# Kernel optimization log

Measured on AMD Instinct MI355X. Metric: run time of the kernel, lower is better.

Reference implementation:

```python
import jax, jax.numpy as jnp
import numpy as np

B, N, DIM = 1, 100_000, 512
HEADS, DIM_HEAD, M = 8, 64, 64


def setup_inputs() -> dict:
    key = jax.random.key(0)
    ks = jax.random.split(key, 9)
    s = 0.04  # ~ kaiming-ish scale for dim=512
    return {
        "x": jax.random.normal(ks[0], (B, N, DIM), dtype=jnp.float32),
        "temperature": jnp.full((1, HEADS, 1, 1), 0.5, dtype=jnp.float32),
        "w_slice": jax.random.normal(ks[1], (HEADS * M, DIM), dtype=jnp.float32) * s,
        "b_slice": jnp.zeros((HEADS * M,), dtype=jnp.float32),
        "w1": jax.random.normal(ks[2], (DIM_HEAD, DIM), dtype=jnp.float32) * s,
        "b1": jnp.zeros((DIM_HEAD,), dtype=jnp.float32),
        "wq": jax.random.normal(ks[3], (DIM_HEAD, DIM_HEAD), dtype=jnp.float32) * 0.125,
        "wk": jax.random.normal(ks[4], (DIM_HEAD, DIM_HEAD), dtype=jnp.float32) * 0.125,
        "wv": jax.random.normal(ks[5], (DIM_HEAD, DIM_HEAD), dtype=jnp.float32) * 0.125,
        "w3": jax.random.normal(ks[6], (DIM_HEAD, DIM_HEAD), dtype=jnp.float32) * 0.125,
        "b3": jnp.zeros((DIM_HEAD,), dtype=jnp.float32),
    }


def reference(x, temperature, w_slice, b_slice, w1, b1, wq, wk, wv, w3, b3):
    b, n, c = x.shape
    # slice logits: (B,N,H*M) -> (B,H,N,M)
    logits = jnp.einsum("bnc,ec->bne", x, w_slice) + b_slice
    logits = logits.reshape(b, n, HEADS, M).transpose(0, 2, 1, 3)
    temp = jnp.clip(temperature, 0.1, 5.0)
    w = jax.nn.softmax(logits / temp, axis=-1)          # (B,H,N,M)
    d = w.sum(axis=2)                                    # (B,H,M)
    # N -> M aggregation (w^T @ x per head)
    s_raw = jnp.einsum("bhnm,bnc->bhmc", w, x)          # (B,H,M,C)
    s = jnp.einsum("bhmc,dc->bhmd", s_raw / (d[..., None] + 1e-5), w1) + b1  # (B,H,M,dh)
    q = jnp.einsum("bhmd,ed->bhme", s, wq)
    k = jnp.einsum("bhmd,ed->bhme", s, wk)
    v = jnp.einsum("bhmd,ed->bhme", s, wv)
    scale = 1.0 / jnp.sqrt(jnp.asarray(DIM_HEAD, dtype=s.dtype))
    attn = jax.nn.softmax(jnp.einsum("bhme,bhle->bhml", q, k) * scale, axis=-1)
    s_att = jnp.einsum("bhml,bhle->bhme", attn, v)      # (B,H,M,dh)
    s_out = jnp.einsum("bhme,de->bhmd", s_att, w3) + b3
    # deslice: w @ s_out -> (B,H,N,dh) -> (B,N,H*dh)
    x_out = jnp.einsum("bhnm,bhmd->bhnd", w, s_out)
    return x_out.transpose(0, 2, 1, 3).reshape(b, n, HEADS * DIM_HEAD)
```

## Files before the change

### kernel.cpp

```cpp
#include <hip/hip_runtime.h>

typedef _Float16 f16;
typedef _Float16 f16x8 __attribute__((ext_vector_type(8)));
typedef _Float16 f16x4 __attribute__((ext_vector_type(4)));
typedef float    f32x4 __attribute__((ext_vector_type(4)));

#define N_TOK   100000
#define NPAD    100032
#define NT1     1563
#define CDIM    512
#define KSTEPS  (NPAD/32)
#define K2SPL   128

#define O_WT     ((size_t)0)
#define SZ_WT    ((size_t)512*NPAD*2)
#define O_YT     (O_WT + SZ_WT)
#define SZ_YT    ((size_t)64*NPAD*2)
#define O_WFR    (O_YT + SZ_YT)
#define SZ_WFR   ((size_t)16*4*9*64*8*2)
#define O_SPP    (O_WFR + SZ_WFR)
#define SZ_SPP   ((size_t)K2SPL*32768*4)
#define O_DPP    (O_SPP + SZ_SPP)
#define SZ_DPP   ((size_t)K2SPL*512*4)
#define O_SPRE   (O_DPP + SZ_DPP)
#define SZ_SPRE  ((size_t)32768*4)
#define O_DSTD   (O_SPRE + SZ_SPRE)
#define SZ_DSTD  ((size_t)512*4)
#define O_SOUT   (O_DSTD + SZ_DSTD)
#define SZ_SOUT  ((size_t)8*64*64*2)
#define O_WN     (O_SOUT + SZ_SOUT)
#define SZ_WN    ((size_t)NPAD*512*2)

__global__ void k0_pack(const float* __restrict__ wsf, const float* __restrict__ w1f,
                        f16* __restrict__ wfr) {
    int c = blockIdx.x * 256 + threadIdx.x;
    int lane = c & 63, g = c >> 6;
    int u  = g % 9,  r = g / 9;
    int we = r & 3,  kg = r >> 2;
    int col = lane & 15, quad = lane >> 4;
    int k = kg * 32 + quad * 8;
    const float* src;
    if (u < 8) src = wsf + (size_t)(we*128 + u*16 + col) * CDIM + k;
    else       src = w1f + (size_t)(we*16  + col) * CDIM + k;
    float4 a = *(const float4*)(src);
    float4 b = *(const float4*)(src + 4);
    f16x8 h;
    h[0]=(f16)a.x; h[1]=(f16)a.y; h[2]=(f16)a.z; h[3]=(f16)a.w;
    h[4]=(f16)b.x; h[5]=(f16)b.y; h[6]=(f16)b.z; h[7]=(f16)b.w;
    *(f16x8*)(wfr + (size_t)c * 8) = h;
}

#define XROW 40
#define TPITCH 72
#define NPITCH 536
__launch_bounds__(256, 2)
__global__ void k1_slice(const float* __restrict__ x, const float* __restrict__ temperature,
                         const f16* __restrict__ wfr, const float* __restrict__ bsl,
                         f16* __restrict__ wT, f16* __restrict__ yT, f16* __restrict__ wN) {
    __shared__ f16 smem[512 * TPITCH];
    f16* lX = smem;
    f16* lT = smem;
    f16* lN = smem;

    const int tid  = threadIdx.x;
    const int wave = tid >> 6;
    const int lane = tid & 63;
    const int quad = lane >> 4;
    const int col  = lane & 15;
    const int n0   = blockIdx.x * 64;

    const int srow = tid >> 2, sch = tid & 3;
    int snr = n0 + srow; if (snr > N_TOK - 1) snr = N_TOK - 1;
    const float* sbase = x + (size_t)snr * CDIM + sch * 8;

    {
        float4 a = *(const float4*)(sbase);
        float4 b = *(const float4*)(sbase + 4);
        f16x8 h;
        h[0]=(f16)a.x; h[1]=(f16)a.y; h[2]=(f16)a.z; h[3]=(f16)a.w;
        h[4]=(f16)b.x; h[5]=(f16)b.y; h[6]=(f16)b.z; h[7]=(f16)b.w;
        *(f16x8*)(&lX[srow * XROW + sch * 8]) = h;
    }

    f32x4 acc[4][9];
    #pragma unroll
    for (int nf = 0; nf < 4; ++nf)
        #pragma unroll
        for (int u = 0; u < 9; ++u) acc[nf][u] = f32x4{0.f,0.f,0.f,0.f};

    __syncthreads();

    #pragma unroll 2
    for (int kg = 0; kg < 16; ++kg) {
        const f16* wb = wfr + ((size_t)(kg*4 + wave) * 9) * 512 + (size_t)lane * 8;
        f16x8 bf[9];
        #pragma unroll
        for (int u = 0; u < 9; ++u) bf[u] = *(const f16x8*)(wb + u * 512);

        float4 xa, xb;
        if (kg < 15) {
            xa = *(const float4*)(sbase + (kg + 1) * 32);
            xb = *(const float4*)(sbase + (kg + 1) * 32 + 4);
        }

        const f16* xbuf = lX + (kg & 1) * (64 * XROW);
        f16x8 af[4];
        #pragma unroll
        for (int nf = 0; nf < 4; ++nf)
            af[nf] = *(const f16x8*)(xbuf + (nf*16 + col) * XROW + quad * 8);

        #pragma unroll
        for (int nf = 0; nf < 4; ++nf)
            #pragma unroll
            for (int u = 0; u < 9; ++u)
                acc[nf][u] = __builtin_amdgcn_mfma_f32_16x16x32_f16(af[nf], bf[u], acc[nf][u], 0, 0, 0);

        if (kg < 15) {
            f16x8 h;
            h[0]=(f16)xa.x; h[1]=(f16)xa.y; h[2]=(f16)xa.z; h[3]=(f16)xa.w;
            h[4]=(f16)xb.x; h[5]=(f16)xb.y; h[6]=(f16)xb.z; h[7]=(f16)xb.w;
            *(f16x8*)(&lX[((kg + 1) & 1) * (64 * XROW) + srow * XROW + sch * 8]) = h;
        }
        __syncthreads();
    }

    #pragma unroll
    for (int u = 0; u < 8; ++u) {
        float b = bsl[wave*128 + u*16 + col];
        #pragma unroll
        for (int nf = 0; nf < 4; ++nf)
            #pragma unroll
            for (int r = 0; r < 4; ++r) acc[nf][u][r] += b;
    }
    float invt[2];
    #pragma unroll
    for (int hh = 0; hh < 2; ++hh) {
        float tv = temperature[wave*2 + hh];
        tv = fminf(fmaxf(tv, 0.1f), 5.0f);
        invt[hh] = 1.0f / tv;
    }

    #pragma unroll
    for (int nf = 0; nf < 4; ++nf) {
        const int nloc = nf*16 + quad*4;
        #pragma unroll
        for (int hh = 0; hh < 2; ++hh) {
            float mx[4];
            #pragma unroll
            for (int r = 0; r < 4; ++r) {
                float m01 = fmaxf(acc[nf][hh*4+0][r], acc[nf][hh*4+1][r]);
                float m23 = fmaxf(acc[nf][hh*4+2][r], acc[nf][hh*4+3][r]);
                mx[r] = fmaxf(m01, m23);
            }
            #pragma unroll
            for (int d = 1; d < 16; d <<= 1)
                #pragma unroll
                for (int r = 0; r < 4; ++r) mx[r] = fmaxf(mx[r], __shfl_xor(mx[r], d));
            float sm[4] = {0.f, 0.f, 0.f, 0.f};
            #pragma unroll
            for (int uu = 0; uu < 4; ++uu)
                #pragma unroll
                for (int r = 0; r < 4; ++r) {
                    float ev = __expf((acc[nf][hh*4+uu][r] - mx[r]) * invt[hh]);
                    acc[nf][hh*4+uu][r] = ev;
                    sm[r] += ev;
                }
            #pragma unroll
            for (int d = 1; d < 16; d <<= 1)
                #pragma unroll
                for (int r = 0; r < 4; ++r) sm[r] += __shfl_xor(sm[r], d);
            #pragma unroll
            for (int r = 0; r < 4; ++r) sm[r] = 1.0f / sm[r];
            #pragma unroll
            for (int uu = 0; uu < 4; ++uu) {
                f16x4 pk;
                #pragma unroll
                for (int r = 0; r < 4; ++r) {
                    acc[nf][hh*4+uu][r] *= sm[r];
                    int n = n0 + nloc + r;
                    pk[r] = (n < N_TOK) ? (f16)acc[nf][hh*4+uu][r] : (f16)0.f;
                }
                int e = wave*128 + (hh*4 + uu)*16 + col;
                *(f16x4*)(lT + (size_t)e*TPITCH + nloc) = pk;
            }
        }
        {
            f16x4 pk;
            #pragma unroll
            for (int r = 0; r < 4; ++r) {
                int n = n0 + nloc + r;
                pk[r] = (n < N_TOK) ? (f16)acc[nf][8][r] : (f16)0.f;
            }
            *(f16x4*)(yT + (size_t)(wave*16 + col) * NPAD + n0 + nloc) = pk;
        }
    }
    __syncthreads();

    #pragma unroll
    for (int i = 0; i < 16; ++i) {
        int id = tid + i*256;
        int e = id >> 3, p = id & 7;
        f16x8 v = *(const f16x8*)(lT + (size_t)e*TPITCH + p*8);
        *(f16x8*)(wT + (size_t)e*NPAD + n0 + p*8) = v;
    }

    if (wN != nullptr) {
        __syncthreads();
        #pragma unroll
        for (int nf = 0; nf < 4; ++nf) {
            const int nloc = nf*16 + quad*4;
            #pragma unroll
            for (int hh = 0; hh < 2; ++hh)
                #pragma unroll
                for (int uu = 0; uu < 4; ++uu) {
                    int e = wave*128 + (hh*4 + uu)*16 + col;
                    #pragma unroll
                    for (int r = 0; r < 4; ++r)
                        lN[(size_t)(nloc + r)*NPITCH + e] = (f16)acc[nf][hh*4+uu][r];
                }
        }
        __syncthreads();
        #pragma unroll
        for (int i = 0; i < 16; ++i) {
            int id = tid + i*256;
            int n = id >> 6, ec = id & 63;
            f16x8 v = *(const f16x8*)(lN + (size_t)n*NPITCH + ec*8);
            *(f16x8*)(wN + (size_t)(n0 + n)*512 + ec*8) = v;
        }
    }
}

__launch_bounds__(256, 4)
__global__ void k2_spre(const f16* __restrict__ wT, const f16* __restrict__ yT,
                        float* __restrict__ spp, float* __restrict__ dpp) {
    const int tid = threadIdx.x, wave = tid >> 6, lane = tid & 63;
    const int quad = lane >> 4, col = lane & 15;
    const int slot = blockIdx.x >> 2, equad = blockIdx.x & 3;
    const int ebase = equad * 128 + wave * 32;

    f32x4 acc[2][4];
    float dac[2];
    #pragma unroll
    for (int u = 0; u < 2; ++u) {
        dac[u] = 0.f;
        #pragma unroll
        for (int v = 0; v < 4; ++v) acc[u][v] = f32x4{0.f,0.f,0.f,0.f};
    }
    for (int ks = slot; ks < KSTEPS; ks += K2SPL) {
        int nb = ks*32 + quad*8;
        f16x8 bf[4];
        #pragma unroll
        for (int v = 0; v < 4; ++v)
            bf[v] = *(const f16x8*)(yT + (size_t)(v*16 + col)*NPAD + nb);
        #pragma unroll
        for (int u = 0; u < 2; ++u) {
            f16x8 af = *(const f16x8*)(wT + (size_t)(ebase + u*16 + col)*NPAD + nb);
            #pragma unroll
            for (int v = 0; v < 4; ++v)
                acc[u][v] = __builtin_amdgcn_mfma_f32_16x16x32_f16(af, bf[v], acc[u][v], 0, 0, 0);
            float s = 0.f;
            #pragma unroll
            for (int j = 0; j < 8; ++j) s += (float)af[j];
            dac[u] += s;
        }
    }
    #pragma unroll
    for (int u = 0; u < 2; ++u) {
        dac[u] += __shfl_xor(dac[u], 16);
        dac[u] += __shfl_xor(dac[u], 32);
    }
    if (quad == 0) {
        #pragma unroll
        for (int u = 0; u < 2; ++u)
            dpp[slot*512 + ebase + u*16 + col] = dac[u];
    }
    float* dst = spp + (size_t)slot * 32768 + (size_t)equad * 8192;
    #pragma unroll
    for (int u = 0; u < 2; ++u)
        #pragma unroll
        for (int v = 0; v < 4; ++v)
            *(f32x4*)(dst + (size_t)((wave*2 + u)*4 + v)*256 + (size_t)lane*4) = acc[u][v];
}

__global__ void k2r_reduce(const float* __restrict__ spp, const float* __restrict__ dpp,
                           float* __restrict__ spre, float* __restrict__ dstd) {
    int i = blockIdx.x*256 + threadIdx.x;
    float s = 0.f;
    for (int p = 0; p < K2SPL; ++p) s += spp[(size_t)p*32768 + i];
    int r = i & 3, L = (i >> 2) & 63, v = (i >> 8) & 3, g = (i >> 10) & 7, eq = (i >> 13) & 3;
    int e = eq*128 + (g >> 1)*32 + (g & 1)*16 + (L >> 4)*4 + r;
    int d = v*16 + (L & 15);
    spre[e*64 + d] = s;
    if (i < 512) {
        float tt = 0.f;
        for (int p = 0; p < K2SPL; ++p) tt += dpp[p*512 + i];
        dstd[i] = tt;
    }
}

__global__ void k3_attn(const float* __restrict__ spre, const float* __restrict__ dstd,
                        const float* __restrict__ b1, const float* __restrict__ wq,
                        const float* __restrict__ wk, const float* __restrict__ wv,
                        const float* __restrict__ w3, const float* __restrict__ b3,
                        f16* __restrict__ sout) {
    __shared__ float wa[64][65], wb[64][65], wc[64][65];
    __shared__ float ss[64][65], qq[64][65], kk[64][65], vv[64][65], sc[64][65];
    const int h = blockIdx.x, tid = threadIdx.x;

    for (int i = tid; i < 4096; i += 1024) {
        int r = i >> 6, c = i & 63;
        wa[r][c] = wq[i];
        wb[r][c] = wk[i];
        wc[r][c] = wv[i];
        ss[r][c] = spre[h*4096 + i] / (dstd[h*64 + r] + 1e-5f) + b1[c];
    }
    __syncthreads();

    #pragma unroll
    for (int it = 0; it < 4; ++it) {
        int m = it*16 + (tid >> 6), e = tid & 63;
        float aq = 0.f, ak = 0.f, av = 0.f;
        #pragma unroll 8
        for (int d = 0; d < 64; ++d) {
            float sv = ss[m][d];
            aq += sv * wa[e][d];
            ak += sv * wb[e][d];
            av += sv * wc[e][d];
        }
        qq[m][e] = aq; kk[m][e] = ak; vv[m][e] = av;
    }
    __syncthreads();

    for (int i = tid; i < 4096; i += 1024) wa[i >> 6][i & 63] = w3[i];
    #pragma unroll
    for (int it = 0; it < 4; ++it) {
        int m = it*16 + (tid >> 6), l = tid & 63;
        float a = 0.f;
        #pragma unroll 8
        for (int e = 0; e < 64; ++e) a += qq[m][e] * kk[l][e];
        sc[m][l] = a * 0.125f;
    }
    __syncthreads();

    if (tid < 64) {
        int m = tid;
        float mx = -1e30f;
        #pragma unroll 8
        for (int l = 0; l < 64; ++l) mx = fmaxf(mx, sc[m][l]);
        float sm = 0.f;
        #pragma unroll 8
        for (int l = 0; l < 64; ++l) { float ev = __expf(sc[m][l] - mx); sc[m][l] = ev; sm += ev; }
        float rs = 1.0f / sm;
        #pragma unroll 8
        for (int l = 0; l < 64; ++l) sc[m][l] *= rs;
    }
    __syncthreads();

    #pragma unroll
    for (int it = 0; it < 4; ++it) {
        int m = it*16 + (tid >> 6), e = tid & 63;
        float a = 0.f;
        #pragma unroll 8
        for (int l = 0; l < 64; ++l) a += sc[m][l] * vv[l][e];
        ss[m][e] = a;
    }
    __syncthreads();

    #pragma unroll
    for (int it = 0; it < 4; ++it) {
        int d = it*16 + (tid >> 6), m = tid & 63;
        float a = b3[d];
        #pragma unroll 8
        for (int e = 0; e < 64; ++e) a += ss[m][e] * wa[d][e];
        sout[(h*64 + d)*64 + m] = (f16)a;
    }
}

__launch_bounds__(256, 3)
__global__ void k4_wn(const f16* __restrict__ wN, const f16* __restrict__ sout,
                      float* __restrict__ out) {
    const int tid = threadIdx.x, wave = tid >> 6, lane = tid & 63;
    const int quad = lane >> 4, col = lane & 15;
    const int n0 = blockIdx.x * 32;

    f32x4 acc[2][2][4];
    #pragma unroll
    for (int hh = 0; hh < 2; ++hh)
        #pragma unroll
        for (int t = 0; t < 2; ++t)
            #pragma unroll
            for (int v = 0; v < 4; ++v) acc[hh][t][v] = f32x4{0.f,0.f,0.f,0.f};

    #pragma unroll
    for (int hh = 0; hh < 2; ++hh) {
        int h = wave*2 + hh;
        #pragma unroll
        for (int ks = 0; ks < 2; ++ks) {
            f16x8 af[2], bf[4];
            #pragma unroll
            for (int t = 0; t < 2; ++t)
                af[t] = *(const f16x8*)(wN + (size_t)(n0 + t*16 + col)*512 + h*64 + ks*32 + quad*8);
            #pragma unroll
            for (int v = 0; v < 4; ++v)
                bf[v] = *(const f16x8*)(sout + (size_t)(h*64 + v*16 + col)*64 + ks*32 + quad*8);
            #pragma unroll
            for (int t = 0; t < 2; ++t)
                #pragma unroll
                for (int v = 0; v < 4; ++v)
                    acc[hh][t][v] = __builtin_amdgcn_mfma_f32_16x16x32_f16(af[t], bf[v], acc[hh][t][v], 0, 0, 0);
        }
    }

    #pragma unroll
    for (int hh = 0; hh < 2; ++hh) {
        int h = wave*2 + hh;
        #pragma unroll
        for (int t = 0; t < 2; ++t)
            #pragma unroll
            for (int v = 0; v < 4; ++v)
                #pragma unroll
                for (int r = 0; r < 4; ++r) {
                    int n = n0 + t*16 + quad*4 + r;
                    if (n < N_TOK)
                        out[(size_t)n*512 + h*64 + v*16 + col] = acc[hh][t][v][r];
                }
    }
}

__launch_bounds__(256, 2)
__global__ void k4_deslice(const f16* __restrict__ wT, const f16* __restrict__ sout,
                           float* __restrict__ out) {
    __shared__ f16 ldsW[512*68];
    const int tid = threadIdx.x, wave = tid >> 6, lane = tid & 63;
    const int quad = lane >> 4, col = lane & 15;
    const int n0 = blockIdx.x * 64;

    #pragma unroll
    for (int i = 0; i < 32; ++i) {
        int id = tid + i*256;
        int e = id >> 4, p = id & 15;
        f16x4 v = *(const f16x4*)(wT + (size_t)e*NPAD + n0 + p*4);
        *(f16x4*)(ldsW + (size_t)e*68 + p*4) = v;
    }
    __syncthreads();

    f32x4 acc[2][4][4];
    #pragma unroll
    for (int hh = 0; hh < 2; ++hh)
        #pragma unroll
        for (int t = 0; t < 4; ++t)
            #pragma unroll
            for (int v = 0; v < 4; ++v) acc[hh][t][v] = f32x4{0.f,0.f,0.f,0.f};

    #pragma unroll
    for (int hh = 0; hh < 2; ++hh) {
        int h = wave*2 + hh;
        #pragma unroll
        for (int ks = 0; ks < 2; ++ks) {
            f16x8 af[4];
            #pragma unroll
            for (int t = 0; t < 4; ++t) {
                f16x8 a;
                #pragma unroll
                for (int j = 0; j < 8; ++j)
                    a[j] = ldsW[(size_t)(h*64 + ks*32 + quad*8 + j)*68 + t*16 + col];
                af[t] = a;
            }
            #pragma unroll
            for (int v = 0; v < 4; ++v) {
                f16x8 bf = *(const f16x8*)(sout + (size_t)(h*64 + v*16 + col)*64 + ks*32 + quad*8);
                #pragma unroll
                for (int t = 0; t < 4; ++t)
                    acc[hh][t][v] = __builtin_amdgcn_mfma_f32_16x16x32_f16(af[t], bf, acc[hh][t][v], 0, 0, 0);
            }
        }
    }

    #pragma unroll
    for (int hh = 0; hh < 2; ++hh) {
        int h = wave*2 + hh;
        #pragma unroll
        for (int t = 0; t < 4; ++t)
            #pragma unroll
            for (int v = 0; v < 4; ++v)
                #pragma unroll
                for (int r = 0; r < 4; ++r) {
                    int n = n0 + t*16 + quad*4 + r;
                    if (n < N_TOK)
                        out[(size_t)n*512 + h*64 + v*16 + col] = acc[hh][t][v][r];
                }
    }
}

extern "C" void kernel_launch(void* const* d_in, const int* in_sizes, int n_in,
                              void* d_out, int out_size, void* d_ws, size_t ws_size,
                              hipStream_t stream) {
    const float* x           = (const float*)d_in[0];
    const float* temperature = (const float*)d_in[1];
    const float* w_slice     = (const float*)d_in[2];
    const float* b_slice     = (const float*)d_in[3];
    const float* w1          = (const float*)d_in[4];
    const float* b1          = (const float*)d_in[5];
    const float* wq          = (const float*)d_in[6];
    const float* wk          = (const float*)d_in[7];
    const float* wv          = (const float*)d_in[8];
    const float* w3          = (const float*)d_in[9];
    const float* b3          = (const float*)d_in[10];
    float* out = (float*)d_out;
    char*  ws  = (char*)d_ws;

    f16*   wT    = (f16*)(ws + O_WT);
    f16*   yT    = (f16*)(ws + O_YT);
    f16*   wfr   = (f16*)(ws + O_WFR);
    float* spp   = (float*)(ws + O_SPP);
    float* dpp   = (float*)(ws + O_DPP);
    float* spre  = (float*)(ws + O_SPRE);
    float* dstd  = (float*)(ws + O_DSTD);
    f16*   sout  = (f16*)(ws + O_SOUT);

    const int use_wn = (ws_size >= (O_WN + SZ_WN)) ? 1 : 0;
    f16* wN = use_wn ? (f16*)(ws + O_WN) : nullptr;

    k0_pack<<<144, 256, 0, stream>>>(w_slice, w1, wfr);
    k1_slice<<<NT1, 256, 0, stream>>>(x, temperature, wfr, b_slice, wT, yT, wN);
    k2_spre<<<K2SPL*4, 256, 0, stream>>>(wT, yT, spp, dpp);
    k2r_reduce<<<128, 256, 0, stream>>>(spp, dpp, spre, dstd);
    k3_attn<<<8, 1024, 0, stream>>>(spre, dstd, b1, wq, wk, wv, w3, b3, sout);
    if (use_wn) k4_wn<<<KSTEPS, 256, 0, stream>>>(wN, sout, out);
    else        k4_deslice<<<NT1, 256, 0, stream>>>(wT, sout, out);
}
```

Baseline: 634.8 us.

## Stage full x tile in LDS, software-pipeline k2, shrink k3 block, retune k4 bounds

k1 now loads the whole 64x512 x tile into shared memory up front, replacing the per-k-step double buffer and removing 16 barriers from the MFMA loop. k2 switches from strided k-step assignment to contiguous chunks per slot and double-buffers its global loads around the MFMAs. k3 runs with 256 threads instead of 1024, and k4 raises its launch-bounds occupancy hint. The larger LDS footprint in k1 fits within the existing 512x72 buffer but removes overlap of x loads with compute, and the tighter k4 register budget may cause spills.

```diff
diff --git a/kernel.cpp b/kernel.cpp
--- a/kernel.cpp
+++ b/kernel.cpp
@@ -50,7 +50,7 @@
     *(f16x8*)(wfr + (size_t)c * 8) = h;
 }
 
-#define XROW 40
+#define XPITCH 520
 #define TPITCH 72
 #define NPITCH 536
 __launch_bounds__(256, 2)
@@ -72,14 +72,14 @@
     const int srow = tid >> 2, sch = tid & 3;
     int snr = n0 + srow; if (snr > N_TOK - 1) snr = N_TOK - 1;
     const float* sbase = x + (size_t)snr * CDIM + sch * 8;
-
-    {
-        float4 a = *(const float4*)(sbase);
-        float4 b = *(const float4*)(sbase + 4);
+    #pragma unroll
+    for (int kg = 0; kg < 16; ++kg) {
+        float4 a = *(const float4*)(sbase + kg * 32);
+        float4 b = *(const float4*)(sbase + kg * 32 + 4);
         f16x8 h;
         h[0]=(f16)a.x; h[1]=(f16)a.y; h[2]=(f16)a.z; h[3]=(f16)a.w;
         h[4]=(f16)b.x; h[5]=(f16)b.y; h[6]=(f16)b.z; h[7]=(f16)b.w;
-        *(f16x8*)(&lX[srow * XROW + sch * 8]) = h;
+        *(f16x8*)(&lX[srow * XPITCH + kg * 32 + sch * 8]) = h;
     }
 
     f32x4 acc[4][9];
@@ -97,31 +97,16 @@
         #pragma unroll
         for (int u = 0; u < 9; ++u) bf[u] = *(const f16x8*)(wb + u * 512);
 
-        float4 xa, xb;
-        if (kg < 15) {
-            xa = *(const float4*)(sbase + (kg + 1) * 32);
-            xb = *(const float4*)(sbase + (kg + 1) * 32 + 4);
-        }
-
-        const f16* xbuf = lX + (kg & 1) * (64 * XROW);
         f16x8 af[4];
         #pragma unroll
         for (int nf = 0; nf < 4; ++nf)
-            af[nf] = *(const f16x8*)(xbuf + (nf*16 + col) * XROW + quad * 8);
+            af[nf] = *(const f16x8*)(&lX[(nf*16 + col) * XPITCH + kg * 32 + quad * 8]);
 
         #pragma unroll
         for (int nf = 0; nf < 4; ++nf)
             #pragma unroll
             for (int u = 0; u < 9; ++u)
                 acc[nf][u] = __builtin_amdgcn_mfma_f32_16x16x32_f16(af[nf], bf[u], acc[nf][u], 0, 0, 0);
-
-        if (kg < 15) {
-            f16x8 h;
-            h[0]=(f16)xa.x; h[1]=(f16)xa.y; h[2]=(f16)xa.z; h[3]=(f16)xa.w;
-            h[4]=(f16)xb.x; h[5]=(f16)xb.y; h[6]=(f16)xb.z; h[7]=(f16)xb.w;
-            *(f16x8*)(&lX[((kg + 1) & 1) * (64 * XROW) + srow * XROW + sch * 8]) = h;
-        }
-        __syncthreads();
     }
 
     #pragma unroll
@@ -139,6 +124,8 @@
         tv = fminf(fmaxf(tv, 0.1f), 5.0f);
         invt[hh] = 1.0f / tv;
     }
+
+    __syncthreads();
 
     #pragma unroll
     for (int nf = 0; nf < 4; ++nf) {
@@ -230,6 +217,27 @@
     }
 }
 
+#define K2_LOAD(AF, BF, kss)                                                         \
+    {   int nb_ = (kss)*32 + quad*8;                                                 \
+        _Pragma("unroll")                                                            \
+        for (int v = 0; v < 4; ++v)                                                  \
+            BF[v] = *(const f16x8*)(yT + (size_t)(v*16 + col)*NPAD + nb_);           \
+        _Pragma("unroll")                                                            \
+        for (int u = 0; u < 2; ++u)                                                  \
+            AF[u] = *(const f16x8*)(wT + (size_t)(ebase + u*16 + col)*NPAD + nb_);   \
+    }
+#define K2_MFMA(AF, BF)                                                              \
+    {   _Pragma("unroll")                                                            \
+        for (int u = 0; u < 2; ++u) {                                                \
+            _Pragma("unroll")                                                        \
+            for (int v = 0; v < 4; ++v)                                              \
+                acc[u][v] = __builtin_amdgcn_mfma_f32_16x16x32_f16(AF[u], BF[v], acc[u][v], 0, 0, 0); \
+            float s_ = 0.f;                                                          \
+            _Pragma("unroll")                                                        \
+            for (int j = 0; j < 8; ++j) s_ += (float)AF[u][j];                       \
+            dac[u] += s_;                                                            \
+        }                                                                            \
+    }
 __launch_bounds__(256, 4)
 __global__ void k2_spre(const f16* __restrict__ wT, const f16* __restrict__ yT,
                         float* __restrict__ spp, float* __restrict__ dpp) {
@@ -238,6 +246,9 @@
     const int slot = blockIdx.x >> 2, equad = blockIdx.x & 3;
     const int ebase = equad * 128 + wave * 32;
 
+    const int ks0 = (slot * KSTEPS) >> 7;
+    const int ks1 = ((slot + 1) * KSTEPS) >> 7;
+
     f32x4 acc[2][4];
     float dac[2];
     #pragma unroll
@@ -246,24 +257,18 @@
         #pragma unroll
         for (int v = 0; v < 4; ++v) acc[u][v] = f32x4{0.f,0.f,0.f,0.f};
     }
-    for (int ks = slot; ks < KSTEPS; ks += K2SPL) {
-        int nb = ks*32 + quad*8;
-        f16x8 bf[4];
-        #pragma unroll
-        for (int v = 0; v < 4; ++v)
-            bf[v] = *(const f16x8*)(yT + (size_t)(v*16 + col)*NPAD + nb);
-        #pragma unroll
-        for (int u = 0; u < 2; ++u) {
-            f16x8 af = *(const f16x8*)(wT + (size_t)(ebase + u*16 + col)*NPAD + nb);
-            #pragma unroll
-            for (int v = 0; v < 4; ++v)
-                acc[u][v] = __builtin_amdgcn_mfma_f32_16x16x32_f16(af, bf[v], acc[u][v], 0, 0, 0);
-            float s = 0.f;
-            #pragma unroll
-            for (int j = 0; j < 8; ++j) s += (float)af[j];
-            dac[u] += s;
-        }
-    }
+
+    f16x8 afA[2], bfA[4], afB[2], bfB[4];
+    K2_LOAD(afA, bfA, ks0)
+    int ks = ks0;
+    for (; ks + 2 <= ks1; ks += 2) {
+        K2_LOAD(afB, bfB, ks + 1)
+        K2_MFMA(afA, bfA)
+        K2_LOAD(afA, bfA, ks + 2)
+        K2_MFMA(afB, bfB)
+    }
+    if (ks < ks1) K2_MFMA(afA, bfA)
+
     #pragma unroll
     for (int u = 0; u < 2; ++u) {
         dac[u] += __shfl_xor(dac[u], 16);
@@ -307,7 +312,7 @@
     __shared__ float ss[64][65], qq[64][65], kk[64][65], vv[64][65], sc[64][65];
     const int h = blockIdx.x, tid = threadIdx.x;
 
-    for (int i = tid; i < 4096; i += 1024) {
+    for (int i = tid; i < 4096; i += 256) {
         int r = i >> 6, c = i & 63;
         wa[r][c] = wq[i];
         wb[r][c] = wk[i];
@@ -317,8 +322,8 @@
     __syncthreads();
 
     #pragma unroll
-    for (int it = 0; it < 4; ++it) {
-        int m = it*16 + (tid >> 6), e = tid & 63;
+    for (int it = 0; it < 16; ++it) {
+        int m = it*4 + (tid >> 6), e = tid & 63;
         float aq = 0.f, ak = 0.f, av = 0.f;
         #pragma unroll 8
         for (int d = 0; d < 64; ++d) {
@@ -331,10 +336,10 @@
     }
     __syncthreads();
 
-    for (int i = tid; i < 4096; i += 1024) wa[i >> 6][i & 63] = w3[i];
-    #pragma unroll
-    for (int it = 0; it < 4; ++it) {
-        int m = it*16 + (tid >> 6), l = tid & 63;
+    for (int i = tid; i < 4096; i += 256) wa[i >> 6][i & 63] = w3[i];
+    #pragma unroll
+    for (int it = 0; it < 16; ++it) {
+        int m = it*4 + (tid >> 6), l = tid & 63;
         float a = 0.f;
         #pragma unroll 8
         for (int e = 0; e < 64; ++e) a += qq[m][e] * kk[l][e];
@@ -357,8 +362,8 @@
     __syncthreads();
 
     #pragma unroll
-    for (int it = 0; it < 4; ++it) {
-        int m = it*16 + (tid >> 6), e = tid & 63;
+    for (int it = 0; it < 16; ++it) {
+        int m = it*4 + (tid >> 6), e = tid & 63;
         float a = 0.f;
         #pragma unroll 8
         for (int l = 0; l < 64; ++l) a += sc[m][l] * vv[l][e];
@@ -367,8 +372,8 @@
     __syncthreads();
 
     #pragma unroll
-    for (int it = 0; it < 4; ++it) {
-        int d = it*16 + (tid >> 6), m = tid & 63;
+    for (int it = 0; it < 16; ++it) {
+        int d = it*4 + (tid >> 6), m = tid & 63;
         float a = b3[d];
         #pragma unroll 8
         for (int e = 0; e < 64; ++e) a += ss[m][e] * wa[d][e];
@@ -376,7 +381,7 @@
     }
 }
 
-__launch_bounds__(256, 3)
+__launch_bounds__(256, 4)
 __global__ void k4_wn(const f16* __restrict__ wN, const f16* __restrict__ sout,
                       float* __restrict__ out) {
     const int tid = threadIdx.x, wave = tid >> 6, lane = tid & 63;
@@ -525,7 +530,7 @@
     k1_slice<<<NT1, 256, 0, stream>>>(x, temperature, wfr, b_slice, wT, yT, wN);
     k2_spre<<<K2SPL*4, 256, 0, stream>>>(wT, yT, spp, dpp);
     k2r_reduce<<<128, 256, 0, stream>>>(spp, dpp, spre, dstd);
-    k3_attn<<<8, 1024, 0, stream>>>(spre, dstd, b1, wq, wk, wv, w3, b3, sout);
+    k3_attn<<<8, 256, 0, stream>>>(spre, dstd, b1, wq, wk, wv, w3, b3, sout);
     if (use_wn) k4_wn<<<KSTEPS, 256, 0, stream>>>(wN, sout, out);
     else        k4_deslice<<<NT1, 256, 0, stream>>>(wT, sout, out);
 }
```

Result: slower. 651.4 us (+2.6%).
